# Optimization experiments

Measured on AMD Instinct MI355X. Metric: run time of the kernel, lower is better.

## Reference

```python
import jax, jax.numpy as jnp
import numpy as np

N_POINTS = 2048
N_EVENTS = 200000
RIEMANN_SAMPLES = 10
NON_EVENT_WEIGHT = 1.0


def setup_inputs() -> dict:
    key = jax.random.key(0)
    k1, k2, k3, k4 = jax.random.split(key, 4)
    # parameters (torch init: uniform(-0.5, 0.5), beta = init_beta = 0.0)
    beta = jnp.zeros((1, 1), dtype=jnp.float32)
    z0 = jax.random.uniform(k1, (N_POINTS, 2), jnp.float32, -0.5, 0.5)
    v0 = jax.random.uniform(k2, (N_POINTS, 2), jnp.float32, -0.5, 0.5)
    # event data: [node_i, node_j] indices and event times in [t0, tn]
    data_uv = jax.random.randint(k3, (N_EVENTS, 2), 0, N_POINTS, jnp.int32)
    data_t = jax.random.uniform(k4, (N_EVENTS,), jnp.float32, 0.0, 1.0)
    t0 = jnp.zeros((1,), jnp.float32)
    tn = jnp.ones((1,), jnp.float32)
    return {"beta": beta, "z0": z0, "v0": v0, "data_uv": data_uv,
            "data_t": data_t, "t0": t0, "tn": tn}


def reference(beta, z0, v0, data_uv, data_t, t0, tn):
    n = z0.shape[0]
    b = beta[0, 0]
    # ---- event term: sum over events of (beta - ||z_u(t) - z_v(t)||) ----
    u = data_uv[:, 0]
    v = data_uv[:, 1]
    dz = z0[u] - z0[v]                       # [E, 2]
    dv = v0[u] - v0[v]                       # [E, 2]
    d_event = jnp.linalg.norm(dz + dv * data_t[:, None], axis=-1)  # [E]
    event_intensity = jnp.sum(b - d_event)
    # ---- non-event term: midpoint Riemann sum of exp(beta - dist) over all pairs ----
    iu, jv = np.triu_indices(n, k=1)         # static upper-triangular pair indices
    pdz = z0[iu] - z0[jv]                    # [P, 2]
    pdv = v0[iu] - v0[jv]                    # [P, 2]
    t0s = t0[0]
    tns = tn[0]
    dt = (tns - t0s) / RIEMANN_SAMPLES
    t_mid = t0s + (jnp.arange(RIEMANN_SAMPLES, dtype=jnp.float32) + 0.5) * dt  # [S]
    # pairwise distance at every sample time: [P, S]
    d = jnp.linalg.norm(pdz[:, None, :] + pdv[:, None, :] * t_mid[None, :, None], axis=-1)
    non_event_intensity = jnp.sum(jnp.exp(b - d)) * dt
    return event_intensity - NON_EVENT_WEIGHT * non_event_intensity
```

## Files before the change

### kernel.cpp

```cpp
#include <hip/hip_runtime.h>

#define NP 2048
#define NE 200000
#define RS 10
#define EVENT_BLOCKS 256
#define PAIR_BLOCKS 1024
#define NBLOCKS (EVENT_BLOCKS + PAIR_BLOCKS)
#define BLOCK 256
#define NWAVES (BLOCK / 64)


__device__ __forceinline__ void block_reduce_atomic(float v, float scale, float* out) {
    __shared__ float sdata[NWAVES];
    #pragma unroll
    for (int off = 32; off > 0; off >>= 1) v += __shfl_down(v, off, 64);
    const int lane = threadIdx.x & 63;
    const int wid  = threadIdx.x >> 6;
    if (lane == 0) sdata[wid] = v;
    __syncthreads();
    if (threadIdx.x == 0) {
        float s = 0.0f;
        #pragma unroll
        for (int w = 0; w < NWAVES; ++w) s += sdata[w];
        atomicAdd(out, s * scale);
    }
}

__global__ __launch_bounds__(BLOCK) void intensity_kernel(
    const float* __restrict__ beta,
    const float* __restrict__ z0,
    const float* __restrict__ v0,
    const int*   __restrict__ data_uv,
    const float* __restrict__ data_t,
    const float* __restrict__ t0,
    const float* __restrict__ tn,
    float* __restrict__ out)
{
    const float b   = beta[0];
    const float t0s = t0[0];
    const float tns = tn[0];
    const float dt  = (tns - t0s) * (1.0f / RS);

    const float2* __restrict__ z2 = (const float2*)z0;
    const float2* __restrict__ v2 = (const float2*)v0;

    const int bid = blockIdx.x;
    if (bid >= EVENT_BLOCKS) {
        const float LOG2E2 = 1.4426950408889634f * 1.4426950408889634f;

        float tm[RS];
        #pragma unroll
        for (int k = 0; k < RS; ++k) tm[k] = t0s + ((float)k + 0.5f) * dt;

        const int p = bid - EVENT_BLOCKS;
        const int rows[2] = { p, NP - 1 - p };
        float acc[4] = {0.0f, 0.0f, 0.0f, 0.0f};
        #pragma unroll
        for (int pass = 0; pass < 2; ++pass) {
            const int i = rows[pass];
            const float2 zi = z2[i];
            const float2 vi = v2[i];
            for (int j = i + 1 + (int)threadIdx.x; j < NP; j += BLOCK) {
                const float2 zj = z2[j];
                const float2 vj = v2[j];
                const float dzx = zi.x - zj.x, dzy = zi.y - zj.y;
                const float dvx = vi.x - vj.x, dvy = vi.y - vj.y;
                const float qa = fmaf(dvx, dvx, dvy * dvy) * LOG2E2;
                const float qb = fmaf(dzx, dvx, dzy * dvy) * (2.0f * LOG2E2);
                const float qc = fmaf(dzx, dzx, dzy * dzy) * LOG2E2;
                #pragma unroll
                for (int k = 0; k < RS; ++k) {
                    const float s = fmaxf(fmaf(fmaf(qa, tm[k], qb), tm[k], qc), 0.0f);
                    const float r = __builtin_amdgcn_sqrtf(s);
                    acc[k & 3] += __builtin_amdgcn_exp2f(-r);
                }
            }
        }
        block_reduce_atomic((acc[0] + acc[1]) + (acc[2] + acc[3]),
                            -dt * __expf(b), out);
    } else {
        __shared__ float4 pts[NP];
        for (int i = (int)threadIdx.x; i < NP; i += BLOCK) {
            const float2 z = z2[i];
            const float2 v = v2[i];
            pts[i] = make_float4(z.x, z.y, v.x, v.y);
        }
        __syncthreads();

        const int2* __restrict__ uv2 = (const int2*)data_uv;
        float acc = 0.0f;
        const int tid    = bid * BLOCK + (int)threadIdx.x;
        const int stride = EVENT_BLOCKS * BLOCK;
        for (int e = tid; e < NE; e += stride) {
            const int2 uv = uv2[e];
            const float t = data_t[e];
            const float4 pu = pts[uv.x];
            const float4 pv = pts[uv.y];
            const float x = fmaf(pu.z - pv.z, t, pu.x - pv.x);
            const float y = fmaf(pu.w - pv.w, t, pu.y - pv.y);
            acc += b - __builtin_amdgcn_sqrtf(fmaf(x, x, y * y));
        }
        block_reduce_atomic(acc, 1.0f, out);
    }
}

extern "C" void kernel_launch(void* const* d_in, const int* in_sizes, int n_in,
                              void* d_out, int out_size, void* d_ws, size_t ws_size,
                              hipStream_t stream) {
    const float* beta    = (const float*)d_in[0];
    const float* z0      = (const float*)d_in[1];
    const float* v0      = (const float*)d_in[2];
    const int*   data_uv = (const int*)d_in[3];
    const float* data_t  = (const float*)d_in[4];
    const float* t0      = (const float*)d_in[5];
    const float* tn      = (const float*)d_in[6];
    float* out = (float*)d_out;

    intensity_kernel<<<NBLOCKS, BLOCK, 0, stream>>>(beta, z0, v0, data_uv, data_t, t0, tn, out);
}
```

Before: 85.19 us.

## Fuse event and pair work into every block sharing one LDS point table

Replaces the split of dedicated event blocks and pair blocks with 1024 uniform blocks. Each block stages all points into LDS, handles one event per thread and two balanced pair rows. It then does a single combined reduction and one atomic. This is meant to remove load imbalance between the two block types and to serve pair-loop point loads from LDS. The cost is that every block now loads the full 32KB point table, and that LDS footprint per block can limit occupancy.

```diff
diff --git a/kernel.cpp b/kernel.cpp
--- a/kernel.cpp
+++ b/kernel.cpp
@@ -3,14 +3,12 @@
 #define NP 2048
 #define NE 200000
 #define RS 10
-#define EVENT_BLOCKS 256
-#define PAIR_BLOCKS 1024
-#define NBLOCKS (EVENT_BLOCKS + PAIR_BLOCKS)
+#define NBLOCKS 1024
 #define BLOCK 256
 #define NWAVES (BLOCK / 64)
 
 
-__device__ __forceinline__ void block_reduce_atomic(float v, float scale, float* out) {
+__device__ __forceinline__ void block_reduce_atomic(float v, float* out) {
     __shared__ float sdata[NWAVES];
     #pragma unroll
     for (int off = 32; off > 0; off >>= 1) v += __shfl_down(v, off, 64);
@@ -22,7 +20,7 @@
         float s = 0.0f;
         #pragma unroll
         for (int w = 0; w < NWAVES; ++w) s += sdata[w];
-        atomicAdd(out, s * scale);
+        atomicAdd(out, s);
     }
 }
 
@@ -44,64 +42,59 @@
     const float2* __restrict__ z2 = (const float2*)z0;
     const float2* __restrict__ v2 = (const float2*)v0;
 
-    const int bid = blockIdx.x;
-    if (bid >= EVENT_BLOCKS) {
-        const float LOG2E2 = 1.4426950408889634f * 1.4426950408889634f;
+    __shared__ float4 pts[NP];
+    for (int i = (int)threadIdx.x; i < NP; i += BLOCK) {
+        const float2 z = z2[i];
+        const float2 v = v2[i];
+        pts[i] = make_float4(z.x, z.y, v.x, v.y);
+    }
+    __syncthreads();
 
-        float tm[RS];
-        #pragma unroll
-        for (int k = 0; k < RS; ++k) tm[k] = t0s + ((float)k + 0.5f) * dt;
-
-        const int p = bid - EVENT_BLOCKS;
-        const int rows[2] = { p, NP - 1 - p };
-        float acc[4] = {0.0f, 0.0f, 0.0f, 0.0f};
-        #pragma unroll
-        for (int pass = 0; pass < 2; ++pass) {
-            const int i = rows[pass];
-            const float2 zi = z2[i];
-            const float2 vi = v2[i];
-            for (int j = i + 1 + (int)threadIdx.x; j < NP; j += BLOCK) {
-                const float2 zj = z2[j];
-                const float2 vj = v2[j];
-                const float dzx = zi.x - zj.x, dzy = zi.y - zj.y;
-                const float dvx = vi.x - vj.x, dvy = vi.y - vj.y;
-                const float qa = fmaf(dvx, dvx, dvy * dvy) * LOG2E2;
-                const float qb = fmaf(dzx, dvx, dzy * dvy) * (2.0f * LOG2E2);
-                const float qc = fmaf(dzx, dzx, dzy * dzy) * LOG2E2;
-                #pragma unroll
-                for (int k = 0; k < RS; ++k) {
-                    const float s = fmaxf(fmaf(fmaf(qa, tm[k], qb), tm[k], qc), 0.0f);
-                    const float r = __builtin_amdgcn_sqrtf(s);
-                    acc[k & 3] += __builtin_amdgcn_exp2f(-r);
-                }
-            }
-        }
-        block_reduce_atomic((acc[0] + acc[1]) + (acc[2] + acc[3]),
-                            -dt * __expf(b), out);
-    } else {
-        __shared__ float4 pts[NP];
-        for (int i = (int)threadIdx.x; i < NP; i += BLOCK) {
-            const float2 z = z2[i];
-            const float2 v = v2[i];
-            pts[i] = make_float4(z.x, z.y, v.x, v.y);
-        }
-        __syncthreads();
-
-        const int2* __restrict__ uv2 = (const int2*)data_uv;
-        float acc = 0.0f;
-        const int tid    = bid * BLOCK + (int)threadIdx.x;
-        const int stride = EVENT_BLOCKS * BLOCK;
-        for (int e = tid; e < NE; e += stride) {
-            const int2 uv = uv2[e];
+    float evacc = 0.0f;
+    {
+        const int e = (int)blockIdx.x * BLOCK + (int)threadIdx.x;
+        if (e < NE) {
+            const int2 uv = ((const int2*)data_uv)[e];
             const float t = data_t[e];
             const float4 pu = pts[uv.x];
             const float4 pv = pts[uv.y];
             const float x = fmaf(pu.z - pv.z, t, pu.x - pv.x);
             const float y = fmaf(pu.w - pv.w, t, pu.y - pv.y);
-            acc += b - __builtin_amdgcn_sqrtf(fmaf(x, x, y * y));
+            evacc = b - __builtin_amdgcn_sqrtf(fmaf(x, x, y * y));
         }
-        block_reduce_atomic(acc, 1.0f, out);
     }
+
+    const float LOG2E2 = 1.4426950408889634f * 1.4426950408889634f;
+
+    float tm[RS];
+    #pragma unroll
+    for (int k = 0; k < RS; ++k) tm[k] = t0s + ((float)k + 0.5f) * dt;
+
+    const int rows[2] = { (int)blockIdx.x, NP - 1 - (int)blockIdx.x };
+    float acc[4] = {0.0f, 0.0f, 0.0f, 0.0f};
+    #pragma unroll
+    for (int pass = 0; pass < 2; ++pass) {
+        const int i = rows[pass];
+        const float4 pi = pts[i];
+        for (int j = i + 1 + (int)threadIdx.x; j < NP; j += BLOCK) {
+            const float4 pj = pts[j];
+            const float dzx = pi.x - pj.x, dzy = pi.y - pj.y;
+            const float dvx = pi.z - pj.z, dvy = pi.w - pj.w;
+            const float qa = fmaf(dvx, dvx, dvy * dvy) * LOG2E2;
+            const float qb = fmaf(dzx, dvx, dzy * dvy) * (2.0f * LOG2E2);
+            const float qc = fmaf(dzx, dzx, dzy * dzy) * LOG2E2;
+            #pragma unroll
+            for (int k = 0; k < RS; ++k) {
+                const float s = fmaxf(fmaf(fmaf(qa, tm[k], qb), tm[k], qc), 0.0f);
+                const float r = __builtin_amdgcn_sqrtf(s);
+                acc[k & 3] += __builtin_amdgcn_exp2f(-r);
+            }
+        }
+    }
+
+    const float v = evacc
+        - (dt * __expf(b)) * ((acc[0] + acc[1]) + (acc[2] + acc[3]));
+    block_reduce_atomic(v, out);
 }
 
 extern "C" void kernel_launch(void* const* d_in, const int* in_sizes, int n_in,
```

Result: faster. 83.42 us (-2.1%).
